# Optimization experiments

Hardware: AMD Instinct MI355X
Metric: run time of the kernel (lower is better)

The kernel has to match this reference:

```python
import jax, jax.numpy as jnp
import numpy as np

Q_DIM = 1024
KV_DIM = 1024
D_ATTN = 1024
N_HEADS = 16
HDIM = D_ATTN // N_HEADS
LOOKBACK = 3
KW = LOOKBACK + 1
SCALE = HDIM ** -0.5

B, LQ, LKV = 4, 4096, 512


def setup_inputs() -> dict:
    key = jax.random.key(0)
    ks = jax.random.split(key, 6)
    q = jax.random.normal(ks[0], (B, LQ, Q_DIM), dtype=jnp.float32)
    kv_src = jax.random.normal(ks[1], (B, LKV, KV_DIM), dtype=jnp.float32)
    seg_id = jnp.sort(jax.random.randint(ks[2], (B, LQ), 0, LKV), axis=-1)
    # Linear weights (torch convention: y = x @ W.T), no bias
    Wq = jax.random.normal(ks[3], (D_ATTN, Q_DIM), dtype=jnp.float32) * (Q_DIM ** -0.5)
    Wkv = jax.random.normal(ks[4], (2 * D_ATTN, KV_DIM), dtype=jnp.float32) * (KV_DIM ** -0.5)
    Wo = jax.random.normal(ks[5], (Q_DIM, D_ATTN), dtype=jnp.float32) * (D_ATTN ** -0.5)
    return {"q": q, "kv_src": kv_src, "seg_id": seg_id, "Wq": Wq, "Wkv": Wkv, "Wo": Wo}


def _split_heads(x):
    # (B, L, D) -> (B, H, L, Dh)
    b, l, _ = x.shape
    return x.reshape(b, l, N_HEADS, HDIM).transpose(0, 2, 1, 3)


def reference(q, kv_src, seg_id, Wq, Wkv, Wo):
    b, lq, _ = q.shape
    lkv = kv_src.shape[1]

    qh = _split_heads(q @ Wq.T)                      # (B,H,Lq,Dh)
    kv = kv_src @ Wkv.T                              # (B,Lkv,2*D)
    k, v = jnp.split(kv, 2, axis=-1)
    kh = _split_heads(k)                             # (B,H,Lkv,Dh)
    vh = _split_heads(v)

    offsets = jnp.arange(KW)                         # (Kw,)
    gather = seg_id[:, :, None] - offsets            # (B,Lq,Kw)
    neg_mask = gather < 0
    gc = jnp.clip(gather, 0, lkv - 1)                # (B,Lq,Kw)

    b_idx = jnp.arange(b)[:, None, None]
    # advanced indexing: (B,Lq,Kw,H,Dh) -> transpose to (B,H,Lq,Kw,Dh)
    k_sel = kh[b_idx, :, gc].transpose(0, 3, 1, 2, 4)
    v_sel = vh[b_idx, :, gc].transpose(0, 3, 1, 2, 4)

    scores = jnp.einsum('bhqd,bhqkd->bhqk', qh, k_sel) * SCALE
    neg_inf = jnp.finfo(scores.dtype).min
    scores = jnp.where(neg_mask[:, None, :, :], neg_inf, scores)
    probs = jax.nn.softmax(scores, axis=-1)
    out = jnp.einsum('bhqk,bhqkd->bhqd', probs, v_sel)   # (B,H,Lq,Dh)
    out = out.transpose(0, 2, 1, 3).reshape(b, lq, D_ATTN)
    return out @ Wo.T                                # (B,Lq,q_dim)
```

## Files before the change

kernel.cpp:

```cpp
#include <hip/hip_runtime.h>
#include <math.h>

#define NH 16
#define HDIM 64
#define D_ATTN 1024
#define KW 4
#define ATT_SCALE 0.125f
#define LKV_C 512
#define LQ_C 4096
#define B_C 4

typedef _Float16 f16;
typedef _Float16 f16x8 __attribute__((ext_vector_type(8)));
typedef _Float16 f16x4 __attribute__((ext_vector_type(4)));
typedef _Float16 f16x2 __attribute__((ext_vector_type(2)));
typedef float f32x4 __attribute__((ext_vector_type(4)));

typedef __attribute__((address_space(3))) unsigned int as3_uint;
typedef __attribute__((address_space(1))) const unsigned int as1_uint;

__device__ __forceinline__ void gld_lds16(const f16* g, f16* l) {
    __builtin_amdgcn_global_load_lds((as1_uint*)g, (as3_uint*)l, 16, 0, 0);
}

__device__ __forceinline__ float dot4_f16(f16x4 a, f16x4 b) {
#if __has_builtin(__builtin_amdgcn_fdot2)
    f16x2 alo = {a.x, a.y}, ahi = {a.z, a.w};
    f16x2 blo = {b.x, b.y}, bhi = {b.z, b.w};
    float p = __builtin_amdgcn_fdot2(alo, blo, 0.f, false);
    return __builtin_amdgcn_fdot2(ahi, bhi, p, false);
#else
    return (float)a.x * (float)b.x + (float)a.y * (float)b.y +
           (float)a.z * (float)b.z + (float)a.w * (float)b.w;
#endif
}

#define SEG_Q   4194304
#define SEG_KV  (SEG_Q + 524288)
#define SEG_WQ  (SEG_KV + 262144)
#define SEG_WKV (SEG_WQ + 524288)
#define SEG_END (SEG_WKV + 262144)

__global__ __launch_bounds__(256) void split_all(const float* __restrict__ q,
                                                 const float* __restrict__ kv,
                                                 const float* __restrict__ Wq,
                                                 const float* __restrict__ Wkv,
                                                 const float* __restrict__ Wo,
                                                 f16* __restrict__ q_hi,
                                                 f16* __restrict__ kvs_hi,
                                                 f16* __restrict__ Wq_hi,
                                                 f16* __restrict__ Wkv_hi,
                                                 f16* __restrict__ Wo_hi) {
    const int i = blockIdx.x * 256 + threadIdx.x;
    const float* src; f16* dst; int base;
    if (i < SEG_Q)        { src = q;   dst = q_hi;   base = 0; }
    else if (i < SEG_KV)  { src = kv;  dst = kvs_hi; base = SEG_Q; }
    else if (i < SEG_WQ)  { src = Wq;  dst = Wq_hi;  base = SEG_KV; }
    else if (i < SEG_WKV) { src = Wkv; dst = Wkv_hi; base = SEG_WQ; }
    else                  { src = Wo;  dst = Wo_hi;  base = SEG_WKV; }
    const int j = i - base;
    float4 v = ((const float4*)src)[j];
    ((f16x4*)dst)[j] = (f16x4){(f16)v.x, (f16)v.y, (f16)v.z, (f16)v.w};
}

template <typename OT>
__global__ __launch_bounds__(256) void gemm_f16(const f16* __restrict__ A,
                                                const f16* __restrict__ B,
                                                OT* __restrict__ C,
                                                int M, int N, int K) {
    __shared__ f16 smem[2 * 128 * 32];
    f16* sA = smem;
    f16* sB = smem + 4096;

    const int t = threadIdx.x;
    const int w = t >> 6;
    const int lane = t & 63;
    const int bm = blockIdx.y * 128;
    const int bn = blockIdx.x * 128;
    const int wm = (w & 1) * 64;
    const int wn = (w >> 1) * 64;

    f32x4 acc[4][4] = {};

    const int frow = lane & 15;
    const int fchunk = lane >> 4;

    const int srow = t >> 2;
    const int chunk = (t & 3) ^ ((t >> 3) & 3);
    const size_t aoff0 = (size_t)(bm + srow) * K + chunk * 8;
    const size_t aoff1 = (size_t)(bm + 64 + srow) * K + chunk * 8;
    const size_t boff0 = (size_t)(bn + srow) * K + chunk * 8;
    const size_t boff1 = (size_t)(bn + 64 + srow) * K + chunk * 8;
    const unsigned loff0 = (w * 64) * 8;
    const unsigned loff1 = (256 + w * 64) * 8;

    gld_lds16(A + aoff0, sA + loff0);  gld_lds16(A + aoff1, sA + loff1);
    gld_lds16(B + boff0, sB + loff0);  gld_lds16(B + boff1, sB + loff1);

    for (int k0 = 0; k0 < K; k0 += 32) {
        __syncthreads();

        f16x8 a[4], b[4];
        #pragma unroll
        for (int i = 0; i < 4; ++i) {
            const int r = wm + i * 16 + frow;
            a[i] = *(const f16x8*)(sA + r * 32 + (fchunk ^ ((r >> 1) & 3)) * 8);
        }
        #pragma unroll
        for (int j = 0; j < 4; ++j) {
            const int r = wn + j * 16 + frow;
            b[j] = *(const f16x8*)(sB + r * 32 + (fchunk ^ ((r >> 1) & 3)) * 8);
        }

        __syncthreads();

        if (k0 + 32 < K) {
            const int kn = k0 + 32;
            gld_lds16(A + aoff0 + kn, sA + loff0);  gld_lds16(A + aoff1 + kn, sA + loff1);
            gld_lds16(B + boff0 + kn, sB + loff0);  gld_lds16(B + boff1 + kn, sB + loff1);
        }

        #pragma unroll
        for (int i = 0; i < 4; ++i)
            #pragma unroll
            for (int j = 0; j < 4; ++j)
                acc[i][j] = __builtin_amdgcn_mfma_f32_16x16x32_f16(a[i], b[j], acc[i][j], 0, 0, 0);
    }

    const int rbase = bm + wm + (lane >> 4) * 4;
    const int cbase = bn + wn + (lane & 15);
    #pragma unroll
    for (int i = 0; i < 4; ++i)
        #pragma unroll
        for (int j = 0; j < 4; ++j)
            #pragma unroll
            for (int r = 0; r < 4; ++r)
                C[(size_t)(rbase + i * 16 + r) * N + cbase + j * 16] = (OT)acc[i][j][r];
}

__device__ __forceinline__ void stage64(const f16* __restrict__ g, size_t row0,
                                        int K, int kcol, f16* l) {
    const int t = threadIdx.x;
    #pragma unroll
    for (int i = 0; i < 2; ++i) {
        const int idx = i * 256 + t;
        const int r = idx >> 3;
        const int qg = (idx & 7) ^ (r & 7);
        gld_lds16(g + (row0 + r) * (size_t)K + kcol + qg * 8, l + idx * 8);
    }
}

#define BAR __builtin_amdgcn_s_barrier()
#define VM6 asm volatile("s_waitcnt vmcnt(6)" ::: "memory")
#define VM8 asm volatile("s_waitcnt vmcnt(8)" ::: "memory")
#define VM0 asm volatile("s_waitcnt vmcnt(0)" ::: "memory")

#define RD_A(S, mh)                                                         \
    { _Pragma("unroll") for (int mi = 0; mi < 2; ++mi) {                    \
        const f16* p = (S) + ((mh) * 64 + mi * 32 + arow) * 64;             \
        a[0][mi] = *(const f16x8*)(p + q0);                                 \
        a[1][mi] = *(const f16x8*)(p + q1); } }

#define RD_B(S, nh)                                                         \
    { _Pragma("unroll") for (int ni = 0; ni < 2; ++ni) {                    \
        const f16* p = (S) + (((nh) * 2 + ni) * 32 + brow) * 64;            \
        b[0][(nh) * 2 + ni] = *(const f16x8*)(p + q0);                      \
        b[1][(nh) * 2 + ni] = *(const f16x8*)(p + q1); } }

#define QUAD(mh, nh)                                                        \
    { _Pragma("unroll") for (int mi = 0; mi < 2; ++mi)                      \
      _Pragma("unroll") for (int ni = 0; ni < 2; ++ni) {                    \
          f32x4& c = acc[(mh) * 2 + mi][(nh) * 2 + ni];                     \
          c = __builtin_amdgcn_mfma_f32_16x16x32_f16(a[0][mi], b[0][(nh) * 2 + ni], c, 0, 0, 0); \
          c = __builtin_amdgcn_mfma_f32_16x16x32_f16(a[1][mi], b[1][(nh) * 2 + ni], c, 0, 0, 0); \
      } }

#define QUAD2(mh)                                                           \
    { __builtin_amdgcn_s_setprio(1); QUAD(mh, 0); QUAD(mh, 1);              \
      __builtin_amdgcn_s_setprio(0); }

template <typename OT>
__global__ __launch_bounds__(256, 2) void gemm128(const f16* __restrict__ A,
                                                  const f16* __restrict__ B,
                                                  OT* __restrict__ C,
                                                  int M, int N, int K) {
    __shared__ __align__(16) f16 smem[4 * 8192];
    f16* const sA0 = smem;
    f16* const sA1 = smem + 8192;
    f16* const sB0 = smem + 16384;
    f16* const sB1 = smem + 24576;

    const int t = threadIdx.x;
    const int lane = t & 63;
    const int w = t >> 6;
    const int wr = w >> 1;
    const int wc = w & 1;
    const int frow = lane & 15;
    const int fc = lane >> 4;

    const int nbx = N >> 7;
    const int nwg = gridDim.x;
    const int wg = (blockIdx.x & 7) * (nwg >> 3) + (blockIdx.x >> 3);
    const int bm = (wg / nbx) << 7;
    const int bn = (wg % nbx) << 7;

    const int arow = wr * 16 + frow;
    const int brow = wc * 16 + frow;
    const int q0 = (fc ^ (frow & 7)) * 8;
    const int q1 = ((4 + fc) ^ (frow & 7)) * 8;

    f32x4 acc[4][4] = {};
    f16x8 a[2][2], b[2][4];

    stage64(A, bm,      K, 0,  sA0);
    stage64(A, bm + 64, K, 0,  sA0 + 4096);
    stage64(B, bn,      K, 0,  sB0);
    stage64(B, bn + 64, K, 0,  sB0 + 4096);
    stage64(A, bm,      K, 64, sA1);
    stage64(A, bm + 64, K, 64, sA1 + 4096);
    stage64(B, bn,      K, 64, sB1);
    stage64(B, bn + 64, K, 64, sB1 + 4096);
    VM8;
    BAR;

    const int NT = K >> 7;
    for (int it = 0; it < NT; ++it) {
        const bool lastit = (it == NT - 1);
        const int kc1 = (it * 2 + 1) << 6;
        const int kc2 = (it * 2 + 2) << 6;
        const int kc3 = (it * 2 + 3) << 6;

        RD_A(sA0, 0); RD_B(sB0, 0); RD_B(sB0, 1);
        if (it > 0) stage64(A, bm + 64, K, kc1, sA1 + 4096);
        BAR; QUAD2(0); BAR;

        RD_A(sA0, 1);
        if (!lastit) {
            stage64(A, bm,      K, kc2, sA0);
            stage64(B, bn,      K, kc2, sB0);
            stage64(B, bn + 64, K, kc2, sB0 + 4096);
            VM6;
        } else {
            VM0;
        }
        BAR; QUAD2(1); BAR;

        RD_A(sA1, 0); RD_B(sB1, 0); RD_B(sB1, 1);
        if (!lastit) stage64(A, bm + 64, K, kc2, sA0 + 4096);
        BAR; QUAD2(0); BAR;

        RD_A(sA1, 1);
        if (!lastit) {
            stage64(A, bm,      K, kc3, sA1);
            stage64(B, bn,      K, kc3, sB1);
            stage64(B, bn + 64, K, kc3, sB1 + 4096);
            VM6;
        }
        BAR; QUAD2(1); BAR;
    }

    const size_t rb = (size_t)bm + wr * 16 + ((lane >> 4) << 2);
    const int cb = bn + wc * 16 + (lane & 15);
    #pragma unroll
    for (int m = 0; m < 4; ++m)
        #pragma unroll
        for (int n = 0; n < 4; ++n)
            #pragma unroll
            for (int rr = 0; rr < 4; ++rr)
                C[(rb + (m >> 1) * 64 + (m & 1) * 32 + rr) * N + cb + n * 32] =
                    (OT)acc[m][n][rr];
}

__global__ __launch_bounds__(256) void attn_kernel(const f16* __restrict__ qh,
                                                   const f16* __restrict__ kvp,
                                                   const int* __restrict__ seg_id,
                                                   f16* __restrict__ attn_o) {
    const int hg = threadIdx.x >> 6;
    const int lane = threadIdx.x & 63;
    const int r0 = blockIdx.x << 2;
    const int hh = lane >> 4;
    const int s  = lane & 15;
    const int dbase = (hg * 4 + hh) * HDIM + 4 * s;
    const int b = r0 >> 12;
    const f16* kvb = kvp + (size_t)b * LKV_C * (2 * D_ATTN);

    int seg[4];
    f16x4 qv[4];
    #pragma unroll
    for (int i = 0; i < 4; ++i) {
        seg[i] = seg_id[r0 + i];
        qv[i] = *(const f16x4*)(qh + (size_t)(r0 + i) * D_ATTN + dbase);
    }

    f16x4 kk[4][KW], vv[4][KW];
    #pragma unroll
    for (int i = 0; i < 4; ++i)
        #pragma unroll
        for (int w = 0; w < KW; ++w) {
            const int j = seg[i] - w;
            if (j >= 0) {
                const f16* base = kvb + (size_t)j * (2 * D_ATTN);
                kk[i][w] = *(const f16x4*)(base + dbase);
                vv[i][w] = *(const f16x4*)(base + D_ATTN + dbase);
            } else {
                kk[i][w] = (f16x4){0, 0, 0, 0};
                vv[i][w] = (f16x4){0, 0, 0, 0};
            }
        }

    float sc[4][KW];
    #pragma unroll
    for (int i = 0; i < 4; ++i)
        #pragma unroll
        for (int w = 0; w < KW; ++w)
            sc[i][w] = dot4_f16(qv[i], kk[i][w]);
    #pragma unroll
    for (int i = 0; i < 4; ++i)
        #pragma unroll
        for (int w = 0; w < KW; ++w) {
            float p = sc[i][w];
            p += __shfl_xor(p, 1);
            p += __shfl_xor(p, 2);
            p += __shfl_xor(p, 4);
            p += __shfl_xor(p, 8);
            sc[i][w] = (seg[i] - w >= 0) ? p * ATT_SCALE : -1e30f;
        }

    #pragma unroll
    for (int i = 0; i < 4; ++i) {
        const float m = fmaxf(fmaxf(sc[i][0], sc[i][1]), fmaxf(sc[i][2], sc[i][3]));
        float e[KW], sum = 0.f;
        #pragma unroll
        for (int w = 0; w < KW; ++w) {
            e[w] = __expf(sc[i][w] - m);
            sum += e[w];
        }
        const float inv = 1.f / sum;

        float ox = 0.f, oy = 0.f, oz = 0.f, ow = 0.f;
        #pragma unroll
        for (int w = 0; w < KW; ++w) {
            const float c = e[w] * inv;
            ox = fmaf(c, (float)vv[i][w].x, ox);
            oy = fmaf(c, (float)vv[i][w].y, oy);
            oz = fmaf(c, (float)vv[i][w].z, oz);
            ow = fmaf(c, (float)vv[i][w].w, ow);
        }
        *(f16x4*)(attn_o + (size_t)(r0 + i) * D_ATTN + dbase) =
            (f16x4){(f16)ox, (f16)oy, (f16)oz, (f16)ow};
    }
}

extern "C" void kernel_launch(void* const* d_in, const int* in_sizes, int n_in,
                              void* d_out, int out_size, void* d_ws, size_t ws_size,
                              hipStream_t stream) {
    const float* q      = (const float*)d_in[0];
    const float* kv_src = (const float*)d_in[1];
    const int*   seg    = (const int*)  d_in[2];
    const float* Wq     = (const float*)d_in[3];
    const float* Wkv    = (const float*)d_in[4];
    const float* Wo     = (const float*)d_in[5];
    float* out = (float*)d_out;

    const int M  = B_C * LQ_C;
    const int Mk = B_C * LKV_C;

    f16* q_hi   = (f16*)d_ws;
    f16* kvs_hi = q_hi   + (size_t)M * D_ATTN;
    f16* Wq_hi  = kvs_hi + (size_t)Mk * 1024;
    f16* Wkv_hi = Wq_hi  + 1024 * 1024;
    f16* Wo_hi  = Wkv_hi + 2048 * 1024;
    f16* kvp    = Wo_hi  + 1024 * 1024;
    f16* attn_o = q_hi;
    f16* qh16   = (f16*)d_out;

    split_all<<<SEG_END / 256, 256, 0, stream>>>(q, kv_src, Wq, Wkv, Wo,
                                                 q_hi, kvs_hi, Wq_hi, Wkv_hi, Wo_hi);

    gemm_f16<f16><<<dim3(2048 / 128, Mk / 128), 256, 0, stream>>>(kvs_hi, Wkv_hi, kvp, Mk, 2048, 1024);
    gemm128<f16><<<(M / 128) * (1024 / 128), 256, 0, stream>>>(q_hi, Wq_hi, qh16, M, 1024, 1024);
    attn_kernel<<<M / 4, 256, 0, stream>>>(qh16, kvp, seg, attn_o);
    gemm128<float><<<(M / 128) * (1024 / 128), 256, 0, stream>>>(attn_o, Wo_hi, out, M, 1024, 1024);
}
```

Baseline: 259.2 us.

## Use 8 waves per block in the 128x128 GEMM to halve per-wave tile

The 128x128 GEMM kernel now runs 512 threads (8 waves in a 2x4 grid) instead of 256, so each wave computes a 64x32 sub-tile with half the accumulators. Each thread issues one async global-to-LDS load per 64-row stage instead of two, and the vmcnt waits are halved to match. The aim is more waves per CU to hide latency and lower register pressure. The trade-off is more barrier participants and less operand reuse per wave.

```diff
diff --git a/kernel.cpp b/kernel.cpp
--- a/kernel.cpp
+++ b/kernel.cpp
@@ -138,52 +138,46 @@
                 C[(size_t)(rbase + i * 16 + r) * N + cbase + j * 16] = (OT)acc[i][j][r];
 }
 
-__device__ __forceinline__ void stage64(const f16* __restrict__ g, size_t row0,
-                                        int K, int kcol, f16* l) {
-    const int t = threadIdx.x;
-    #pragma unroll
-    for (int i = 0; i < 2; ++i) {
-        const int idx = i * 256 + t;
-        const int r = idx >> 3;
-        const int qg = (idx & 7) ^ (r & 7);
-        gld_lds16(g + (row0 + r) * (size_t)K + kcol + qg * 8, l + idx * 8);
-    }
+__device__ __forceinline__ void stage64w(const f16* __restrict__ g, size_t row0,
+                                         int K, int kcol, f16* l) {
+    const int idx = threadIdx.x;
+    const int r = idx >> 3;
+    const int qg = (idx & 7) ^ (r & 7);
+    gld_lds16(g + (row0 + r) * (size_t)K + kcol + qg * 8, l + idx * 8);
 }
 
 #define BAR __builtin_amdgcn_s_barrier()
-#define VM6 asm volatile("s_waitcnt vmcnt(6)" ::: "memory")
-#define VM8 asm volatile("s_waitcnt vmcnt(8)" ::: "memory")
+#define VM3 asm volatile("s_waitcnt vmcnt(3)" ::: "memory")
+#define VM4 asm volatile("s_waitcnt vmcnt(4)" ::: "memory")
 #define VM0 asm volatile("s_waitcnt vmcnt(0)" ::: "memory")
 
-#define RD_A(S, mh)                                                         \
+#define RD_A8(S, mh)                                                        \
     { _Pragma("unroll") for (int mi = 0; mi < 2; ++mi) {                    \
         const f16* p = (S) + ((mh) * 64 + mi * 32 + arow) * 64;             \
         a[0][mi] = *(const f16x8*)(p + q0);                                 \
         a[1][mi] = *(const f16x8*)(p + q1); } }
 
-#define RD_B(S, nh)                                                         \
+#define RD_B8(S)                                                            \
     { _Pragma("unroll") for (int ni = 0; ni < 2; ++ni) {                    \
-        const f16* p = (S) + (((nh) * 2 + ni) * 32 + brow) * 64;            \
-        b[0][(nh) * 2 + ni] = *(const f16x8*)(p + q0);                      \
-        b[1][(nh) * 2 + ni] = *(const f16x8*)(p + q1); } }
-
-#define QUAD(mh, nh)                                                        \
-    { _Pragma("unroll") for (int mi = 0; mi < 2; ++mi)                      \
+        const f16* p = (S) + (ni * 64 + brow) * 64;                         \
+        b[0][ni] = *(const f16x8*)(p + q0);                                 \
+        b[1][ni] = *(const f16x8*)(p + q1); } }
+
+#define QUAD8(mh)                                                           \
+    { __builtin_amdgcn_s_setprio(1);                                        \
+      _Pragma("unroll") for (int mi = 0; mi < 2; ++mi)                      \
       _Pragma("unroll") for (int ni = 0; ni < 2; ++ni) {                    \
-          f32x4& c = acc[(mh) * 2 + mi][(nh) * 2 + ni];                     \
-          c = __builtin_amdgcn_mfma_f32_16x16x32_f16(a[0][mi], b[0][(nh) * 2 + ni], c, 0, 0, 0); \
-          c = __builtin_amdgcn_mfma_f32_16x16x32_f16(a[1][mi], b[1][(nh) * 2 + ni], c, 0, 0, 0); \
-      } }
-
-#define QUAD2(mh)                                                           \
-    { __builtin_amdgcn_s_setprio(1); QUAD(mh, 0); QUAD(mh, 1);              \
+          f32x4& c = acc[(mh) * 2 + mi][ni];                                \
+          c = __builtin_amdgcn_mfma_f32_16x16x32_f16(a[0][mi], b[0][ni], c, 0, 0, 0); \
+          c = __builtin_amdgcn_mfma_f32_16x16x32_f16(a[1][mi], b[1][ni], c, 0, 0, 0); \
+      }                                                                     \
       __builtin_amdgcn_s_setprio(0); }
 
 template <typename OT>
-__global__ __launch_bounds__(256, 2) void gemm128(const f16* __restrict__ A,
-                                                  const f16* __restrict__ B,
-                                                  OT* __restrict__ C,
-                                                  int M, int N, int K) {
+__global__ __launch_bounds__(512, 4) void gemm128x8(const f16* __restrict__ A,
+                                                    const f16* __restrict__ B,
+                                                    OT* __restrict__ C,
+                                                    int M, int N, int K) {
     __shared__ __align__(16) f16 smem[4 * 8192];
     f16* const sA0 = smem;
     f16* const sA1 = smem + 8192;
@@ -193,8 +187,8 @@
     const int t = threadIdx.x;
     const int lane = t & 63;
     const int w = t >> 6;
-    const int wr = w >> 1;
-    const int wc = w & 1;
+    const int wr = w >> 2;
+    const int wc = w & 3;
     const int frow = lane & 15;
     const int fc = lane >> 4;
 
@@ -209,18 +203,18 @@
     const int q0 = (fc ^ (frow & 7)) * 8;
     const int q1 = ((4 + fc) ^ (frow & 7)) * 8;
 
-    f32x4 acc[4][4] = {};
-    f16x8 a[2][2], b[2][4];
-
-    stage64(A, bm,      K, 0,  sA0);
-    stage64(A, bm + 64, K, 0,  sA0 + 4096);
-    stage64(B, bn,      K, 0,  sB0);
-    stage64(B, bn + 64, K, 0,  sB0 + 4096);
-    stage64(A, bm,      K, 64, sA1);
-    stage64(A, bm + 64, K, 64, sA1 + 4096);
-    stage64(B, bn,      K, 64, sB1);
-    stage64(B, bn + 64, K, 64, sB1 + 4096);
-    VM8;
+    f32x4 acc[4][2] = {};
+    f16x8 a[2][2], b[2][2];
+
+    stage64w(A, bm,      K, 0,  sA0);
+    stage64w(A, bm + 64, K, 0,  sA0 + 4096);
+    stage64w(B, bn,      K, 0,  sB0);
+    stage64w(B, bn + 64, K, 0,  sB0 + 4096);
+    stage64w(A, bm,      K, 64, sA1);
+    stage64w(A, bm + 64, K, 64, sA1 + 4096);
+    stage64w(B, bn,      K, 64, sB1);
+    stage64w(B, bn + 64, K, 64, sB1 + 4096);
+    VM4;
     BAR;
 
     const int NT = K >> 7;
@@ -230,33 +224,33 @@
         const int kc2 = (it * 2 + 2) << 6;
         const int kc3 = (it * 2 + 3) << 6;
 
-        RD_A(sA0, 0); RD_B(sB0, 0); RD_B(sB0, 1);
-        if (it > 0) stage64(A, bm + 64, K, kc1, sA1 + 4096);
-        BAR; QUAD2(0); BAR;
-
-        RD_A(sA0, 1);
+        RD_A8(sA0, 0); RD_B8(sB0);
+        if (it > 0) stage64w(A, bm + 64, K, kc1, sA1 + 4096);
+        BAR; QUAD8(0); BAR;
+
+        RD_A8(sA0, 1);
         if (!lastit) {
-            stage64(A, bm,      K, kc2, sA0);
-            stage64(B, bn,      K, kc2, sB0);
-            stage64(B, bn + 64, K, kc2, sB0 + 4096);
-            VM6;
+            stage64w(A, bm,      K, kc2, sA0);
+            stage64w(B, bn,      K, kc2, sB0);
+            stage64w(B, bn + 64, K, kc2, sB0 + 4096);
+            VM3;
         } else {
             VM0;
         }
-        BAR; QUAD2(1); BAR;
-
-        RD_A(sA1, 0); RD_B(sB1, 0); RD_B(sB1, 1);
-        if (!lastit) stage64(A, bm + 64, K, kc2, sA0 + 4096);
-        BAR; QUAD2(0); BAR;
-
-        RD_A(sA1, 1);
+        BAR; QUAD8(1); BAR;
+
+        RD_A8(sA1, 0); RD_B8(sB1);
+        if (!lastit) stage64w(A, bm + 64, K, kc2, sA0 + 4096);
+        BAR; QUAD8(0); BAR;
+
+        RD_A8(sA1, 1);
         if (!lastit) {
-            stage64(A, bm,      K, kc3, sA1);
-            stage64(B, bn,      K, kc3, sB1);
-            stage64(B, bn + 64, K, kc3, sB1 + 4096);
-            VM6;
-        }
-        BAR; QUAD2(1); BAR;
+            stage64w(A, bm,      K, kc3, sA1);
+            stage64w(B, bn,      K, kc3, sB1);
+            stage64w(B, bn + 64, K, kc3, sB1 + 4096);
+            VM3;
+        }
+        BAR; QUAD8(1); BAR;
     }
 
     const size_t rb = (size_t)bm + wr * 16 + ((lane >> 4) << 2);
@@ -264,10 +258,10 @@
     #pragma unroll
     for (int m = 0; m < 4; ++m)
         #pragma unroll
-        for (int n = 0; n < 4; ++n)
+        for (int n = 0; n < 2; ++n)
             #pragma unroll
             for (int rr = 0; rr < 4; ++rr)
-                C[(rb + (m >> 1) * 64 + (m & 1) * 32 + rr) * N + cb + n * 32] =
+                C[(rb + (m >> 1) * 64 + (m & 1) * 32 + rr) * N + cb + n * 64] =
                     (OT)acc[m][n][rr];
 }
 
@@ -378,7 +372,7 @@
                                                  q_hi, kvs_hi, Wq_hi, Wkv_hi, Wo_hi);
 
     gemm_f16<f16><<<dim3(2048 / 128, Mk / 128), 256, 0, stream>>>(kvs_hi, Wkv_hi, kvp, Mk, 2048, 1024);
-    gemm128<f16><<<(M / 128) * (1024 / 128), 256, 0, stream>>>(q_hi, Wq_hi, qh16, M, 1024, 1024);
+    gemm128x8<f16><<<(M / 128) * (1024 / 128), 512, 0, stream>>>(q_hi, Wq_hi, qh16, M, 1024, 1024);
     attn_kernel<<<M / 4, 256, 0, stream>>>(qh16, kvp, seg, attn_o);
-    gemm128<float><<<(M / 128) * (1024 / 128), 256, 0, stream>>>(attn_o, Wo_hi, out, M, 1024, 1024);
-}
+    gemm128x8<float><<<(M / 128) * (1024 / 128), 512, 0, stream>>>(attn_o, Wo_hi, out, M, 1024, 1024);
+}
```

Result: no change. 255.4 us (-1.5%).
